# Performance work log

Hardware: AMD Instinct MI355X
Metric: run time of the kernel (lower is better)

Reference implementation:

```python
import jax, jax.numpy as jnp
import numpy as np

B, T, H, S = 2, 2048, 16, 64
EMB = H * S  # 1024


def layer_norm(x, g, b, eps=1e-5):
    mu = jnp.mean(x, axis=-1, keepdims=True)
    var = jnp.var(x, axis=-1, keepdims=True)
    return (x - mu) * jax.lax.rsqrt(var + eps) * g + b


def setup_inputs() -> dict:
    key = jax.random.key(0)
    ks = jax.random.split(key, 12)
    sc = 0.02
    return {
        "x": jax.random.normal(ks[0], (B, T, EMB), dtype=jnp.float32),
        "Wkqv": jax.random.normal(ks[1], (S, 3 * S), dtype=jnp.float32) * sc,
        "Wproj": jax.random.normal(ks[2], (EMB, EMB), dtype=jnp.float32) * sc,
        "g1": jnp.ones((EMB,), jnp.float32),
        "b1": jnp.zeros((EMB,), jnp.float32),
        "W1": jax.random.normal(ks[3], (EMB, 4 * EMB), dtype=jnp.float32) * sc,
        "bff1": jnp.zeros((4 * EMB,), jnp.float32),
        "W2": jax.random.normal(ks[4], (4 * EMB, EMB), dtype=jnp.float32) * sc,
        "bff2": jnp.zeros((EMB,), jnp.float32),
        "g2": jnp.ones((EMB,), jnp.float32),
        "b2": jnp.zeros((EMB,), jnp.float32),
    }


def reference(x, Wkqv, Wproj, g1, b1, W1, bff1, W2, bff2, g2, b2):
    Bb, Tt, _ = x.shape
    xh = x.reshape(Bb, Tt, H, S)                     # [B,T,H,S]
    kqv = jnp.einsum('bths,sd->bthd', xh, Wkqv)      # [B,T,H,3S], shared per-head weight
    k, q, v = jnp.split(kqv, 3, axis=-1)             # note order: k, q, v
    scores = jnp.einsum('bihk,bjhk->bijh', q, k) / jnp.sqrt(jnp.float32(S))
    att = jax.nn.softmax(scores, axis=2)             # softmax over key dim j
    res = jnp.einsum('btih,bihs->bths', att, v).reshape(Bb, Tt, EMB)
    mha = res @ Wproj                                # Linear(emb, emb, bias=False)
    x = layer_norm(x + mha, g1, b1)
    h = jax.nn.gelu(x @ W1 + bff1, approximate=False)
    ff = h @ W2 + bff2
    return layer_norm(x + ff, g2, b2)
```

## Files before the change

### kernel.cpp

```cpp
#include <hip/hip_runtime.h>
#include <hip/hip_bf16.h>
#include <math.h>

#define B_ 2
#define T_ 2048
#define H_ 16
#define S_ 64
#define EMB 1024
#define FF 4096
#define BT (B_*T_)
#define ROWS (B_*T_*H_)

typedef __attribute__((ext_vector_type(8))) short s16x8;
typedef __attribute__((ext_vector_type(4))) float f32x4;

struct P4 { unsigned short* p[4]; };

__device__ __forceinline__ unsigned short f2b(float f) {
    return __builtin_bit_cast(unsigned short, __float2bfloat16(f));
}
__device__ __forceinline__ float b2f(short u) {
    return __builtin_bit_cast(float, ((unsigned int)(unsigned short)u) << 16);
}

__device__ __forceinline__ void gl_lds16(const void* g, void* l) {
    __builtin_amdgcn_global_load_lds(
        (const __attribute__((address_space(1))) void*)g,
        (__attribute__((address_space(3))) void*)l, 16, 0, 0);
}

__device__ __forceinline__ f32x4 mfma16(s16x8 a, s16x8 b, f32x4 c) {
    return __builtin_amdgcn_mfma_f32_16x16x32_bf16(a, b, c, 0, 0, 0);
}

__global__ __launch_bounds__(256) void kqv_kernel(const float* __restrict__ x,
        const unsigned short* __restrict__ Wqt, unsigned short* __restrict__ K,
        unsigned short* __restrict__ Q, unsigned short* __restrict__ V) {
    const int tid = threadIdx.x;
    const int w = tid >> 6, lane = tid & 63;
    const int l15 = lane & 15, quad = lane >> 4;
    const long r0 = (long)blockIdx.x * 128 + w * 32;

    s16x8 af[2][2];
    #pragma unroll
    for (int mt = 0; mt < 2; ++mt)
        #pragma unroll
        for (int ks = 0; ks < 2; ++ks) {
            const float* xp = x + (r0 + mt*16 + l15) * 64 + ks*32 + quad*8;
            const float4 v0 = *(const float4*)xp;
            const float4 v1 = *(const float4*)(xp + 4);
            s16x8 a;
            a[0] = (short)f2b(v0.x); a[1] = (short)f2b(v0.y);
            a[2] = (short)f2b(v0.z); a[3] = (short)f2b(v0.w);
            a[4] = (short)f2b(v1.x); a[5] = (short)f2b(v1.y);
            a[6] = (short)f2b(v1.z); a[7] = (short)f2b(v1.w);
            af[mt][ks] = a;
        }

    #pragma unroll
    for (int nt = 0; nt < 12; ++nt) {
        const s16x8 b0 = *(const s16x8*)&Wqt[(nt*16 + l15)*64 + quad*8];
        const s16x8 b1 = *(const s16x8*)&Wqt[(nt*16 + l15)*64 + 32 + quad*8];
        f32x4 acc[2] = {};
        #pragma unroll
        for (int mt = 0; mt < 2; ++mt) {
            acc[mt] = mfma16(af[mt][0], b0, acc[mt]);
            acc[mt] = mfma16(af[mt][1], b1, acc[mt]);
        }
        unsigned short* dst = (nt < 4) ? K : (nt < 8) ? Q : V;
        const int c0 = (nt & 3) * 16 + l15;
        #pragma unroll
        for (int mt = 0; mt < 2; ++mt)
            #pragma unroll
            for (int r = 0; r < 4; ++r)
                dst[(r0 + mt*16 + quad*4 + r) * 64 + c0] = f2b(acc[mt][r]);
    }
}

__global__ __launch_bounds__(256) void attn_kernel(const unsigned short* __restrict__ Q,
        const unsigned short* __restrict__ K, const unsigned short* __restrict__ V,
        unsigned short* __restrict__ Po, float* __restrict__ Pl) {
    __shared__ __align__(16) unsigned short Ks[64 * 64];
    __shared__ __align__(16) unsigned short Vt[64 * 64];
    __shared__ __align__(16) unsigned short Ps[4][32 * 72];
    const int tid = threadIdx.x;
    const int w = tid >> 6, lane = tid & 63;
    const int l15 = lane & 15, quad = lane >> 4;
    const int qt = blockIdx.x;
    const int bh = blockIdx.y;
    const int sidx = blockIdx.z;
    const int b = bh >> 4, h = bh & 15;
    const long base = ((long)b * (T_ * H_) + h) * 64;
    const unsigned short* Qp = Q + base;
    const unsigned short* Kp = K + base;
    const unsigned short* Vp = V + base;
    const int q0 = qt * 128;

    s16x8 qf[2][2];
    #pragma unroll
    for (int mt = 0; mt < 2; ++mt)
        #pragma unroll
        for (int ks = 0; ks < 2; ++ks) {
            const s16x8 raw = *(const s16x8*)&Qp[(long)(q0 + w*32 + mt*16 + l15) * 1024 + ks*32 + quad*8];
            s16x8 q;
            #pragma unroll
            for (int j = 0; j < 8; ++j) q[j] = (short)f2b(b2f(raw[j]) * 0.125f);
            qf[mt][ks] = q;
        }

    s16x8 onef;
    #pragma unroll
    for (int j = 0; j < 8; ++j) onef[j] = (short)0x3F80;

    f32x4 oacc[2][4] = {};
    f32x4 lacc[2] = {};

    const int sjp = tid & 31, sd0 = (tid >> 5) * 8;
    const int kt0 = sidx * 16;
    for (int kt = kt0; kt < kt0 + 16; ++kt) {
        __syncthreads();
        #pragma unroll
        for (int i = 0; i < 2; ++i) {
            const int id = i * 256 + tid;
            const int j = id >> 3, dc = id & 7;
            const s16x8 kv = *(const s16x8*)&Kp[(long)(kt*64 + j) * 1024 + dc*8];
            *(s16x8*)&Ks[j*64 + ((dc ^ (j & 7)) * 8)] = kv;
        }
        {
            const int j0 = sjp * 2;
            const s16x8 va = *(const s16x8*)&Vp[(long)(kt*64 + j0)     * 1024 + sd0];
            const s16x8 vb = *(const s16x8*)&Vp[(long)(kt*64 + j0 + 1) * 1024 + sd0];
            const int jc = j0 >> 3;
            #pragma unroll
            for (int ii = 0; ii < 8; ++ii) {
                const unsigned int pk = (unsigned int)(unsigned short)va[ii]
                                      | ((unsigned int)(unsigned short)vb[ii] << 16);
                const int d = sd0 + ii;
                *(unsigned int*)&Vt[d*64 + ((jc ^ (d & 7)) * 8) + (j0 & 7)] = pk;
            }
        }
        __syncthreads();

        f32x4 sT[4][2] = {};
        #pragma unroll
        for (int ks = 0; ks < 2; ++ks)
            #pragma unroll
            for (int jt = 0; jt < 4; ++jt) {
                const int j = jt*16 + l15;
                const s16x8 kf = *(const s16x8*)&Ks[j*64 + (((ks*4 + quad) ^ (l15 & 7)) * 8)];
                sT[jt][0] = mfma16(kf, qf[0][ks], sT[jt][0]);
                sT[jt][1] = mfma16(kf, qf[1][ks], sT[jt][1]);
            }

        #pragma unroll
        for (int jt = 0; jt < 4; ++jt)
            #pragma unroll
            for (int qt2 = 0; qt2 < 2; ++qt2) {
                const float e0 = __expf(sT[jt][qt2][0]);
                const float e1 = __expf(sT[jt][qt2][1]);
                const float e2 = __expf(sT[jt][qt2][2]);
                const float e3 = __expf(sT[jt][qt2][3]);
                uint2 pk;
                pk.x = (unsigned int)f2b(e0) | ((unsigned int)f2b(e1) << 16);
                pk.y = (unsigned int)f2b(e2) | ((unsigned int)f2b(e3) << 16);
                *(uint2*)&Ps[w][(qt2*16 + l15)*72 + jt*16 + quad*4] = pk;
            }

        #pragma unroll
        for (int ks2 = 0; ks2 < 2; ++ks2) {
            s16x8 pf[2];
            pf[0] = *(const s16x8*)&Ps[w][(l15)*72      + ks2*32 + quad*8];
            pf[1] = *(const s16x8*)&Ps[w][(16 + l15)*72 + ks2*32 + quad*8];
            lacc[0] = mfma16(pf[0], onef, lacc[0]);
            lacc[1] = mfma16(pf[1], onef, lacc[1]);
            #pragma unroll
            for (int nt = 0; nt < 4; ++nt) {
                const int d = nt*16 + l15;
                const s16x8 vf = *(const s16x8*)&Vt[d*64 + (((ks2*4 + quad) ^ (d & 7)) * 8)];
                oacc[0][nt] = mfma16(pf[0], vf, oacc[0][nt]);
                oacc[1][nt] = mfma16(pf[1], vf, oacc[1][nt]);
            }
        }
    }

    const long po_row = (long)(sidx * 32 + bh) * T_;
    #pragma unroll
    for (int mt = 0; mt < 2; ++mt) {
        #pragma unroll
        for (int r = 0; r < 4; ++r) {
            const int t = q0 + w*32 + mt*16 + quad*4 + r;
            if (l15 == 0) Pl[po_row + t] = lacc[mt][r];
            #pragma unroll
            for (int nt = 0; nt < 4; ++nt)
                Po[(po_row + t)*64 + nt*16 + l15] = f2b(oacc[mt][nt][r]);
        }
    }
}

__global__ __launch_bounds__(256) void attn_combine(const unsigned short* __restrict__ Po,
        const float* __restrict__ Pl, unsigned short* __restrict__ res) {
    const int idx = blockIdx.x * 256 + threadIdx.x;
    const int d4 = idx & 15, bht = idx >> 4;
    const ushort4 a = ((const ushort4*)Po)[(long)bht * 16 + d4];
    const ushort4 c = ((const ushort4*)Po)[((long)bht + 32L*T_) * 16 + d4];
    const float inv = 1.f / (Pl[bht] + Pl[bht + 32*T_]);
    const int bh = bht >> 11, t = bht & (T_ - 1);
    const int b = bh >> 4, h = bh & 15;
    uint2 o;
    o.x = (unsigned int)f2b((b2f((short)a.x) + b2f((short)c.x)) * inv)
        | ((unsigned int)f2b((b2f((short)a.y) + b2f((short)c.y)) * inv) << 16);
    o.y = (unsigned int)f2b((b2f((short)a.z) + b2f((short)c.z)) * inv)
        | ((unsigned int)f2b((b2f((short)a.w) + b2f((short)c.w)) * inv) << 16);
    *(uint2*)&res[(long)(b * T_ + t) * EMB + h*64 + d4*4] = o;
}

__global__ __launch_bounds__(256) void gemm_gelu(const unsigned short* __restrict__ A,
        const unsigned short* __restrict__ Bt, const float* __restrict__ bias,
        unsigned short* __restrict__ C, int M, int N, int Kd) {
    __shared__ __align__(16) unsigned short As[128 * 32];
    __shared__ __align__(16) unsigned short Bs[128 * 32];
    const int tid = threadIdx.x;
    const int w = tid >> 6, lane = tid & 63;
    const int l15 = lane & 15, quad = lane >> 4;
    const int wm = w >> 1, wn = w & 1;
    const int bn = blockIdx.x, bm = blockIdx.y;
    const int sr = lane >> 2, skq = lane & 3;
    f32x4 acc[4][4] = {};
    const long arow = (long)(bm*128 + w*32 + sr);
    const long brow = (long)(bn*128 + w*32 + sr);

    for (int kt = 0; kt < Kd; kt += 32) {
        gl_lds16(A  + (arow     )*Kd + kt + skq*8, (char*)As + (w*32     )*64 + lane*16);
        gl_lds16(A  + (arow + 16)*Kd + kt + skq*8, (char*)As + (w*32 + 16)*64 + lane*16);
        gl_lds16(Bt + (brow     )*Kd + kt + skq*8, (char*)Bs + (w*32     )*64 + lane*16);
        gl_lds16(Bt + (brow + 16)*Kd + kt + skq*8, (char*)Bs + (w*32 + 16)*64 + lane*16);
        __syncthreads();
        s16x8 af[4], bf[4];
        #pragma unroll
        for (int mt = 0; mt < 4; ++mt)
            af[mt] = *(const s16x8*)&As[(wm*64 + mt*16 + l15)*32 + quad*8];
        #pragma unroll
        for (int nt = 0; nt < 4; ++nt)
            bf[nt] = *(const s16x8*)&Bs[(wn*64 + nt*16 + l15)*32 + quad*8];
        #pragma unroll
        for (int mt = 0; mt < 4; ++mt)
            #pragma unroll
            for (int nt = 0; nt < 4; ++nt)
                acc[mt][nt] = mfma16(af[mt], bf[nt], acc[mt][nt]);
        __syncthreads();
    }

    #pragma unroll
    for (int mt = 0; mt < 4; ++mt) {
        const int row0 = bm*128 + wm*64 + mt*16 + quad*4;
        #pragma unroll
        for (int nt = 0; nt < 4; ++nt) {
            const int col = bn*128 + wn*64 + nt*16 + l15;
            const float bv = bias[col];
            #pragma unroll
            for (int r = 0; r < 4; ++r) {
                float v = acc[mt][nt][r] + bv;
                v = 0.5f * v * (1.f + erff(v * 0.70710678118654752440f));
                C[(long)(row0 + r)*N + col] = f2b(v);
            }
        }
    }
}

__global__ __launch_bounds__(256) void gemm_splitk(const unsigned short* __restrict__ A,
        const unsigned short* __restrict__ Bt, P4 parts, int M, int N, int Kd, int Ks) {
    __shared__ __align__(16) unsigned short As[128 * 32];
    __shared__ __align__(16) unsigned short Bs[128 * 32];
    const int tid = threadIdx.x;
    const int w = tid >> 6, lane = tid & 63;
    const int l15 = lane & 15, quad = lane >> 4;
    const int wm = w >> 1, wn = w & 1;
    const int bn = blockIdx.x, bm = blockIdx.y, s = blockIdx.z;
    const int sr = lane >> 2, skq = lane & 3;
    f32x4 acc[4][4] = {};
    const long arow = (long)(bm*128 + w*32 + sr);
    const long brow = (long)(bn*128 + w*32 + sr);
    const int k0 = s * Ks;

    for (int kt = k0; kt < k0 + Ks; kt += 32) {
        gl_lds16(A  + (arow     )*Kd + kt + skq*8, (char*)As + (w*32     )*64 + lane*16);
        gl_lds16(A  + (arow + 16)*Kd + kt + skq*8, (char*)As + (w*32 + 16)*64 + lane*16);
        gl_lds16(Bt + (brow     )*Kd + kt + skq*8, (char*)Bs + (w*32     )*64 + lane*16);
        gl_lds16(Bt + (brow + 16)*Kd + kt + skq*8, (char*)Bs + (w*32 + 16)*64 + lane*16);
        __syncthreads();
        s16x8 af[4], bf[4];
        #pragma unroll
        for (int mt = 0; mt < 4; ++mt)
            af[mt] = *(const s16x8*)&As[(wm*64 + mt*16 + l15)*32 + quad*8];
        #pragma unroll
        for (int nt = 0; nt < 4; ++nt)
            bf[nt] = *(const s16x8*)&Bs[(wn*64 + nt*16 + l15)*32 + quad*8];
        #pragma unroll
        for (int mt = 0; mt < 4; ++mt)
            #pragma unroll
            for (int nt = 0; nt < 4; ++nt)
                acc[mt][nt] = mfma16(af[mt], bf[nt], acc[mt][nt]);
        __syncthreads();
    }

    unsigned short* Cp = parts.p[s];
    #pragma unroll
    for (int mt = 0; mt < 4; ++mt) {
        const int row0 = bm*128 + wm*64 + mt*16 + quad*4;
        #pragma unroll
        for (int nt = 0; nt < 4; ++nt) {
            const int col = bn*128 + wn*64 + nt*16 + l15;
            #pragma unroll
            for (int r = 0; r < 4; ++r)
                Cp[(long)(row0 + r)*N + col] = f2b(acc[mt][nt][r]);
        }
    }
}

template <int P, int XBF>
__global__ __launch_bounds__(256) void ln_kernel(const void* __restrict__ xa,
        P4 parts, const float* __restrict__ addb, const float* __restrict__ g,
        const float* __restrict__ bia, float* __restrict__ out,
        unsigned short* __restrict__ outb) {
    const int row = blockIdx.x;
    const int tid = threadIdx.x;
    float4 v;
    if (XBF) {
        const ushort4 u = ((const ushort4*)xa)[(long)row * (EMB/4) + tid];
        v.x = b2f((short)u.x); v.y = b2f((short)u.y);
        v.z = b2f((short)u.z); v.w = b2f((short)u.w);
    } else {
        v = ((const float4*)xa)[(long)row * (EMB/4) + tid];
    }
    #pragma unroll
    for (int p = 0; p < P; ++p) {
        const ushort4 u = ((const ushort4*)(parts.p[p] + (long)row * EMB))[tid];
        v.x += b2f((short)u.x); v.y += b2f((short)u.y);
        v.z += b2f((short)u.z); v.w += b2f((short)u.w);
    }
    if (addb) {
        const float4 ab = ((const float4*)addb)[tid];
        v.x += ab.x; v.y += ab.y; v.z += ab.z; v.w += ab.w;
    }
    float s = v.x + v.y + v.z + v.w;
    float ss = v.x * v.x + v.y * v.y + v.z * v.z + v.w * v.w;
    #pragma unroll
    for (int off = 32; off > 0; off >>= 1) {
        s += __shfl_down(s, off, 64);
        ss += __shfl_down(ss, off, 64);
    }
    __shared__ float ls[4], lss[4];
    __shared__ float mean_s, rstd_s;
    const int wid = tid >> 6, lane = tid & 63;
    if (lane == 0) { ls[wid] = s; lss[wid] = ss; }
    __syncthreads();
    if (tid == 0) {
        const float S0 = ls[0] + ls[1] + ls[2] + ls[3];
        const float S2 = lss[0] + lss[1] + lss[2] + lss[3];
        const float mean = S0 * (1.f / EMB);
        const float var = S2 * (1.f / EMB) - mean * mean;
        mean_s = mean;
        rstd_s = rsqrtf(var + 1e-5f);
    }
    __syncthreads();
    const float mean = mean_s, rstd = rstd_s;
    const float4 gg = ((const float4*)g)[tid];
    const float4 bb = ((const float4*)bia)[tid];
    float4 o;
    o.x = (v.x - mean) * rstd * gg.x + bb.x;
    o.y = (v.y - mean) * rstd * gg.y + bb.y;
    o.z = (v.z - mean) * rstd * gg.z + bb.z;
    o.w = (v.w - mean) * rstd * gg.w + bb.w;
    if (out) ((float4*)(out + (long)row * EMB))[tid] = o;
    if (outb) {
        unsigned short* ob = outb + (long)row * EMB + tid * 4;
        ob[0] = f2b(o.x); ob[1] = f2b(o.y); ob[2] = f2b(o.z); ob[3] = f2b(o.w);
    }
}

__global__ __launch_bounds__(256) void transp_all(const float* __restrict__ Wp,
        const float* __restrict__ W1, const float* __restrict__ W2,
        const float* __restrict__ Wq, unsigned short* __restrict__ Wpt,
        unsigned short* __restrict__ W1t, unsigned short* __restrict__ W2t,
        unsigned short* __restrict__ Wqt) {
    int id = blockIdx.x;
    const float* W; unsigned short* Wt; int Kd, N, ntx;
    if (id < 1024)      {            W = Wp; Wt = Wpt; Kd = 1024; N = 1024; ntx = 32; }
    else if (id < 5120) { id -= 1024; W = W1; Wt = W1t; Kd = 1024; N = 4096; ntx = 128; }
    else if (id < 9216) { id -= 5120; W = W2; Wt = W2t; Kd = 4096; N = 1024; ntx = 32; }
    else                { id -= 9216; W = Wq; Wt = Wqt; Kd = 64;   N = 192;  ntx = 6;  }
    __shared__ float Ts[32][33];
    const int tid = threadIdx.x;
    const int n0 = (id % ntx) * 32, k0 = (id / ntx) * 32;
    const int r = tid >> 3, c4 = (tid & 7) * 4;
    const float4 v = *(const float4*)&W[(long)(k0 + r) * N + n0 + c4];
    Ts[r][c4] = v.x; Ts[r][c4 + 1] = v.y; Ts[r][c4 + 2] = v.z; Ts[r][c4 + 3] = v.w;
    __syncthreads();
    #pragma unroll
    for (int i = 0; i < 4; ++i)
        Wt[(long)(n0 + r) * Kd + k0 + c4 + i] = f2b(Ts[c4 + i][r]);
}

extern "C" void kernel_launch(void* const* d_in, const int* in_sizes, int n_in,
                              void* d_out, int out_size, void* d_ws, size_t ws_size,
                              hipStream_t stream) {
    (void)in_sizes; (void)n_in; (void)out_size;
    const float* x     = (const float*)d_in[0];
    const float* Wkqv  = (const float*)d_in[1];
    const float* Wproj = (const float*)d_in[2];
    const float* g1    = (const float*)d_in[3];
    const float* b1    = (const float*)d_in[4];
    const float* W1    = (const float*)d_in[5];
    const float* bff1  = (const float*)d_in[6];
    const float* W2    = (const float*)d_in[7];
    const float* bff2  = (const float*)d_in[8];
    const float* g2    = (const float*)d_in[9];
    const float* b2    = (const float*)d_in[10];
    float* out = (float*)d_out;
    char* ws = (char*)d_ws;

    const size_t MB = 1u << 20;
    unsigned short* Qb   = (unsigned short*)(ws + 0 * MB);
    unsigned short* Kb   = (unsigned short*)(ws + 8 * MB);
    unsigned short* Vb   = (unsigned short*)(ws + 16 * MB);
    unsigned short* resb = (unsigned short*)(ws + 24 * MB);
    unsigned short* hb   = (unsigned short*)(ws + 8 * MB);
    unsigned short* Po   = (unsigned short*)(ws + 40 * MB);
    float*          Pl   = (float*)(ws + 56 * MB);
    unsigned short* mp0  = (unsigned short*)(ws + 40 * MB);
    unsigned short* mp1  = (unsigned short*)(ws + 48 * MB);
    unsigned short* x1b  = Qb;
    unsigned short* Wpt  = (unsigned short*)(ws + 72 * MB);
    unsigned short* W1t  = (unsigned short*)(ws + 74 * MB);
    unsigned short* W2t  = (unsigned short*)(ws + 82 * MB);
    unsigned short* Wqt  = (unsigned short*)(ws + 90 * MB);
    unsigned short* fp2  = (unsigned short*)(ws + 91 * MB);
    unsigned short* fp3  = (unsigned short*)(ws + 99 * MB);
    const bool big = ws_size >= 108 * MB;

    transp_all<<<dim3(9228), 256, 0, stream>>>(Wproj, W1, W2, Wkqv, Wpt, W1t, W2t, Wqt);

    kqv_kernel<<<dim3(ROWS/128), 256, 0, stream>>>(x, Wqt, Kb, Qb, Vb);
    attn_kernel<<<dim3(T_/128, B_*H_, 2), 256, 0, stream>>>(Qb, Kb, Vb, Po, Pl);
    attn_combine<<<dim3(32*T_*16/256), 256, 0, stream>>>(Po, Pl, resb);
    P4 mp; mp.p[0] = mp0; mp.p[1] = mp1; mp.p[2] = nullptr; mp.p[3] = nullptr;
    gemm_splitk<<<dim3(EMB/128, BT/128, 2), 256, 0, stream>>>(resb, Wpt, mp, BT, EMB, EMB, EMB/2);
    ln_kernel<2, 0><<<dim3(BT), 256, 0, stream>>>(x, mp, nullptr, g1, b1, nullptr, x1b);
    gemm_gelu<<<dim3(FF/128, BT/128), 256, 0, stream>>>(x1b, W1t, bff1, hb, BT, FF, EMB);
    if (big) {
        P4 fp; fp.p[0] = mp0; fp.p[1] = mp1; fp.p[2] = fp2; fp.p[3] = fp3;
        gemm_splitk<<<dim3(EMB/128, BT/128, 4), 256, 0, stream>>>(hb, W2t, fp, BT, EMB, FF, FF/4);
        ln_kernel<4, 1><<<dim3(BT), 256, 0, stream>>>(x1b, fp, bff2, g2, b2, out, nullptr);
    } else {
        P4 fp; fp.p[0] = mp0; fp.p[1] = mp1; fp.p[2] = nullptr; fp.p[3] = nullptr;
        gemm_splitk<<<dim3(EMB/128, BT/128, 2), 256, 0, stream>>>(hb, W2t, fp, BT, EMB, FF, FF/2);
        ln_kernel<2, 1><<<dim3(BT), 256, 0, stream>>>(x1b, fp, bff2, g2, b2, out, nullptr);
    }
}
```

Before: 374.3 us.

## Restructure attention into single-wave blocks with async double-buffered K/V staging

Adds a separate kernel that writes V in transposed layout, so attention can stream K and V^T tiles straight into LDS with global_load_lds. Each attention block becomes one wave owning 32 queries. It double-buffers 32-key tiles behind vmcnt waits instead of block-wide barriers, and normalizes the output in-kernel, which removes the split-K partial buffers and the combine kernel. The trade-offs are an extra transpose pass over V, single-wave blocks that rely on occupancy to hide latency, and no barrier between LDS writes and reads other than the vmcnt wait.

```diff
diff --git a/kernel.cpp b/kernel.cpp
--- a/kernel.cpp
+++ b/kernel.cpp
@@ -32,6 +32,9 @@
 __device__ __forceinline__ f32x4 mfma16(s16x8 a, s16x8 b, f32x4 c) {
     return __builtin_amdgcn_mfma_f32_16x16x32_bf16(a, b, c, 0, 0, 0);
 }
+
+#define WAIT_VM8 0x0F78
+#define WAIT_VM0 0x0F70
 
 __global__ __launch_bounds__(256) void kqv_kernel(const float* __restrict__ x,
         const unsigned short* __restrict__ Wqt, unsigned short* __restrict__ K,
@@ -77,35 +80,59 @@
     }
 }
 
-__global__ __launch_bounds__(256) void attn_kernel(const unsigned short* __restrict__ Q,
-        const unsigned short* __restrict__ K, const unsigned short* __restrict__ V,
-        unsigned short* __restrict__ Po, float* __restrict__ Pl) {
-    __shared__ __align__(16) unsigned short Ks[64 * 64];
-    __shared__ __align__(16) unsigned short Vt[64 * 64];
-    __shared__ __align__(16) unsigned short Ps[4][32 * 72];
-    const int tid = threadIdx.x;
-    const int w = tid >> 6, lane = tid & 63;
+__global__ __launch_bounds__(256) void vt_kernel(const unsigned short* __restrict__ V,
+        unsigned short* __restrict__ VT) {
+    __shared__ unsigned short Ts[64][72];
+    const int tid = threadIdx.x;
+    const int tt = blockIdx.x, bh = blockIdx.y;
+    const int b = bh >> 4, h = bh & 15;
+    const long vbase = ((long)b * (T_*H_) + h) * 64;
+    #pragma unroll
+    for (int i = 0; i < 2; ++i) {
+        const int id = i * 256 + tid;
+        const int tr = id >> 3, dc = (id & 7) * 8;
+        const s16x8 v = *(const s16x8*)&V[vbase + (long)(tt*64 + tr)*1024 + dc];
+        *(s16x8*)&Ts[tr][dc] = v;
+    }
+    __syncthreads();
+    #pragma unroll
+    for (int i = 0; i < 2; ++i) {
+        const int id = i * 256 + tid;
+        const int d = id >> 3, tc = (id & 7) * 8;
+        s16x8 o;
+        #pragma unroll
+        for (int j = 0; j < 8; ++j) o[j] = (short)Ts[tc + j][d];
+        *(s16x8*)&VT[((long)bh*64 + d)*2048 + tt*64 + tc] = o;
+    }
+}
+
+__global__ __launch_bounds__(64, 2) void attn_kernel(const unsigned short* __restrict__ Q,
+        const unsigned short* __restrict__ K, const unsigned short* __restrict__ VT,
+        unsigned short* __restrict__ res) {
+    __shared__ __align__(16) unsigned short Kbuf[2][2][32*32];
+    __shared__ __align__(16) unsigned short Vbuf[2][64*32];
+    __shared__ __align__(16) unsigned short Ps[32*36];
+    const int lane = threadIdx.x;
     const int l15 = lane & 15, quad = lane >> 4;
-    const int qt = blockIdx.x;
-    const int bh = blockIdx.y;
-    const int sidx = blockIdx.z;
+    const int bid = blockIdx.x;
+    const int qt = bid & 63, bh = bid >> 6;
     const int b = bh >> 4, h = bh & 15;
-    const long base = ((long)b * (T_ * H_) + h) * 64;
+    const long base = ((long)b * (T_*H_) + h) * 64;
     const unsigned short* Qp = Q + base;
     const unsigned short* Kp = K + base;
-    const unsigned short* Vp = V + base;
-    const int q0 = qt * 128;
+    const unsigned short* Vp = VT + (long)bh * 64 * 2048;
+    const int q0 = qt * 32;
 
     s16x8 qf[2][2];
     #pragma unroll
-    for (int mt = 0; mt < 2; ++mt)
+    for (int qq = 0; qq < 2; ++qq)
         #pragma unroll
         for (int ks = 0; ks < 2; ++ks) {
-            const s16x8 raw = *(const s16x8*)&Qp[(long)(q0 + w*32 + mt*16 + l15) * 1024 + ks*32 + quad*8];
+            const s16x8 raw = *(const s16x8*)&Qp[(long)(q0 + qq*16 + l15)*1024 + ks*32 + quad*8];
             s16x8 q;
             #pragma unroll
             for (int j = 0; j < 8; ++j) q[j] = (short)f2b(b2f(raw[j]) * 0.125f);
-            qf[mt][ks] = q;
+            qf[qq][ks] = q;
         }
 
     s16x8 onef;
@@ -115,103 +142,81 @@
     f32x4 oacc[2][4] = {};
     f32x4 lacc[2] = {};
 
-    const int sjp = tid & 31, sd0 = (tid >> 5) * 8;
-    const int kt0 = sidx * 16;
-    for (int kt = kt0; kt < kt0 + 16; ++kt) {
-        __syncthreads();
-        #pragma unroll
-        for (int i = 0; i < 2; ++i) {
-            const int id = i * 256 + tid;
-            const int j = id >> 3, dc = id & 7;
-            const s16x8 kv = *(const s16x8*)&Kp[(long)(kt*64 + j) * 1024 + dc*8];
-            *(s16x8*)&Ks[j*64 + ((dc ^ (j & 7)) * 8)] = kv;
-        }
-        {
-            const int j0 = sjp * 2;
-            const s16x8 va = *(const s16x8*)&Vp[(long)(kt*64 + j0)     * 1024 + sd0];
-            const s16x8 vb = *(const s16x8*)&Vp[(long)(kt*64 + j0 + 1) * 1024 + sd0];
-            const int jc = j0 >> 3;
-            #pragma unroll
-            for (int ii = 0; ii < 8; ++ii) {
-                const unsigned int pk = (unsigned int)(unsigned short)va[ii]
-                                      | ((unsigned int)(unsigned short)vb[ii] << 16);
-                const int d = sd0 + ii;
-                *(unsigned int*)&Vt[d*64 + ((jc ^ (d & 7)) * 8) + (j0 & 7)] = pk;
-            }
-        }
-        __syncthreads();
-
-        f32x4 sT[4][2] = {};
+    const int j16 = lane >> 2;
+    const int c8  = (lane & 3) * 8;
+
+    auto stage = [&](int bufi, int kt) {
+        const unsigned short* kg = Kp + (long)(kt*32) * 1024;
+        char* kl = (char*)&Kbuf[bufi][0][0];
+        gl_lds16(kg + (long)j16*1024 + c8,           kl +    0 + lane*16);
+        gl_lds16(kg + (long)(j16+16)*1024 + c8,      kl + 1024 + lane*16);
+        gl_lds16(kg + (long)j16*1024 + 32 + c8,      kl + 2048 + lane*16);
+        gl_lds16(kg + (long)(j16+16)*1024 + 32 + c8, kl + 3072 + lane*16);
+        const unsigned short* vg = Vp + kt*32 + c8;
+        char* vl = (char*)&Vbuf[bufi][0];
+        gl_lds16(vg + (long)(j16     )*2048, vl +    0 + lane*16);
+        gl_lds16(vg + (long)(j16 + 16)*2048, vl + 1024 + lane*16);
+        gl_lds16(vg + (long)(j16 + 32)*2048, vl + 2048 + lane*16);
+        gl_lds16(vg + (long)(j16 + 48)*2048, vl + 3072 + lane*16);
+    };
+
+    auto compute = [&](int bufi) {
+        f32x4 sT[2][2] = {};
         #pragma unroll
         for (int ks = 0; ks < 2; ++ks)
             #pragma unroll
-            for (int jt = 0; jt < 4; ++jt) {
-                const int j = jt*16 + l15;
-                const s16x8 kf = *(const s16x8*)&Ks[j*64 + (((ks*4 + quad) ^ (l15 & 7)) * 8)];
+            for (int jt = 0; jt < 2; ++jt) {
+                const s16x8 kf = *(const s16x8*)&Kbuf[bufi][ks][(jt*16 + l15)*32 + quad*8];
                 sT[jt][0] = mfma16(kf, qf[0][ks], sT[jt][0]);
                 sT[jt][1] = mfma16(kf, qf[1][ks], sT[jt][1]);
             }
-
-        #pragma unroll
-        for (int jt = 0; jt < 4; ++jt)
-            #pragma unroll
-            for (int qt2 = 0; qt2 < 2; ++qt2) {
-                const float e0 = __expf(sT[jt][qt2][0]);
-                const float e1 = __expf(sT[jt][qt2][1]);
-                const float e2 = __expf(sT[jt][qt2][2]);
-                const float e3 = __expf(sT[jt][qt2][3]);
+        #pragma unroll
+        for (int jt = 0; jt < 2; ++jt)
+            #pragma unroll
+            for (int qq = 0; qq < 2; ++qq) {
                 uint2 pk;
-                pk.x = (unsigned int)f2b(e0) | ((unsigned int)f2b(e1) << 16);
-                pk.y = (unsigned int)f2b(e2) | ((unsigned int)f2b(e3) << 16);
-                *(uint2*)&Ps[w][(qt2*16 + l15)*72 + jt*16 + quad*4] = pk;
+                pk.x = (unsigned int)f2b(__expf(sT[jt][qq][0]))
+                     | ((unsigned int)f2b(__expf(sT[jt][qq][1])) << 16);
+                pk.y = (unsigned int)f2b(__expf(sT[jt][qq][2]))
+                     | ((unsigned int)f2b(__expf(sT[jt][qq][3])) << 16);
+                *(uint2*)&Ps[(qq*16 + l15)*36 + jt*16 + quad*4] = pk;
             }
-
-        #pragma unroll
-        for (int ks2 = 0; ks2 < 2; ++ks2) {
-            s16x8 pf[2];
-            pf[0] = *(const s16x8*)&Ps[w][(l15)*72      + ks2*32 + quad*8];
-            pf[1] = *(const s16x8*)&Ps[w][(16 + l15)*72 + ks2*32 + quad*8];
-            lacc[0] = mfma16(pf[0], onef, lacc[0]);
-            lacc[1] = mfma16(pf[1], onef, lacc[1]);
-            #pragma unroll
-            for (int nt = 0; nt < 4; ++nt) {
-                const int d = nt*16 + l15;
-                const s16x8 vf = *(const s16x8*)&Vt[d*64 + (((ks2*4 + quad) ^ (d & 7)) * 8)];
-                oacc[0][nt] = mfma16(pf[0], vf, oacc[0][nt]);
-                oacc[1][nt] = mfma16(pf[1], vf, oacc[1][nt]);
-            }
-        }
-    }
-
-    const long po_row = (long)(sidx * 32 + bh) * T_;
-    #pragma unroll
-    for (int mt = 0; mt < 2; ++mt) {
+        s16x8 pf[2];
+        #pragma unroll
+        for (int qq = 0; qq < 2; ++qq) {
+            pf[qq] = *(const s16x8*)&Ps[(qq*16 + l15)*36 + quad*8];
+            lacc[qq] = mfma16(pf[qq], onef, lacc[qq]);
+        }
+        #pragma unroll
+        for (int nt = 0; nt < 4; ++nt) {
+            const s16x8 vf = *(const s16x8*)&Vbuf[bufi][(nt*16 + l15)*32 + quad*8];
+            oacc[0][nt] = mfma16(pf[0], vf, oacc[0][nt]);
+            oacc[1][nt] = mfma16(pf[1], vf, oacc[1][nt]);
+        }
+    };
+
+    stage(0, 0);
+    for (int kt = 0; kt < 63; ++kt) {
+        stage((kt + 1) & 1, kt + 1);
+        __builtin_amdgcn_s_waitcnt(WAIT_VM8);
+        __builtin_amdgcn_sched_barrier(0);
+        compute(kt & 1);
+    }
+    __builtin_amdgcn_s_waitcnt(WAIT_VM0);
+    __builtin_amdgcn_sched_barrier(0);
+    compute(1);
+
+    #pragma unroll
+    for (int qq = 0; qq < 2; ++qq)
         #pragma unroll
         for (int r = 0; r < 4; ++r) {
-            const int t = q0 + w*32 + mt*16 + quad*4 + r;
-            if (l15 == 0) Pl[po_row + t] = lacc[mt][r];
+            const float inv = 1.f / lacc[qq][r];
+            const int t = q0 + qq*16 + quad*4 + r;
             #pragma unroll
             for (int nt = 0; nt < 4; ++nt)
-                Po[(po_row + t)*64 + nt*16 + l15] = f2b(oacc[mt][nt][r]);
-        }
-    }
-}
-
-__global__ __launch_bounds__(256) void attn_combine(const unsigned short* __restrict__ Po,
-        const float* __restrict__ Pl, unsigned short* __restrict__ res) {
-    const int idx = blockIdx.x * 256 + threadIdx.x;
-    const int d4 = idx & 15, bht = idx >> 4;
-    const ushort4 a = ((const ushort4*)Po)[(long)bht * 16 + d4];
-    const ushort4 c = ((const ushort4*)Po)[((long)bht + 32L*T_) * 16 + d4];
-    const float inv = 1.f / (Pl[bht] + Pl[bht + 32*T_]);
-    const int bh = bht >> 11, t = bht & (T_ - 1);
-    const int b = bh >> 4, h = bh & 15;
-    uint2 o;
-    o.x = (unsigned int)f2b((b2f((short)a.x) + b2f((short)c.x)) * inv)
-        | ((unsigned int)f2b((b2f((short)a.y) + b2f((short)c.y)) * inv) << 16);
-    o.y = (unsigned int)f2b((b2f((short)a.z) + b2f((short)c.z)) * inv)
-        | ((unsigned int)f2b((b2f((short)a.w) + b2f((short)c.w)) * inv) << 16);
-    *(uint2*)&res[(long)(b * T_ + t) * EMB + h*64 + d4*4] = o;
+                res[((long)(b*T_ + t))*EMB + h*64 + nt*16 + l15] =
+                    f2b(oacc[qq][nt][r] * inv);
+        }
 }
 
 __global__ __launch_bounds__(256) void gemm_gelu(const unsigned short* __restrict__ A,
@@ -425,8 +430,7 @@
     unsigned short* Vb   = (unsigned short*)(ws + 16 * MB);
     unsigned short* resb = (unsigned short*)(ws + 24 * MB);
     unsigned short* hb   = (unsigned short*)(ws + 8 * MB);
-    unsigned short* Po   = (unsigned short*)(ws + 40 * MB);
-    float*          Pl   = (float*)(ws + 56 * MB);
+    unsigned short* VTb  = (unsigned short*)(ws + 40 * MB);
     unsigned short* mp0  = (unsigned short*)(ws + 40 * MB);
     unsigned short* mp1  = (unsigned short*)(ws + 48 * MB);
     unsigned short* x1b  = Qb;
@@ -441,8 +445,8 @@
     transp_all<<<dim3(9228), 256, 0, stream>>>(Wproj, W1, W2, Wkqv, Wpt, W1t, W2t, Wqt);
 
     kqv_kernel<<<dim3(ROWS/128), 256, 0, stream>>>(x, Wqt, Kb, Qb, Vb);
-    attn_kernel<<<dim3(T_/128, B_*H_, 2), 256, 0, stream>>>(Qb, Kb, Vb, Po, Pl);
-    attn_combine<<<dim3(32*T_*16/256), 256, 0, stream>>>(Po, Pl, resb);
+    vt_kernel<<<dim3(T_/64, B_*H_), 256, 0, stream>>>(Vb, VTb);
+    attn_kernel<<<dim3(2048), 64, 0, stream>>>(Qb, Kb, VTb, resb);
     P4 mp; mp.p[0] = mp0; mp.p[1] = mp1; mp.p[2] = nullptr; mp.p[3] = nullptr;
     gemm_splitk<<<dim3(EMB/128, BT/128, 2), 256, 0, stream>>>(resb, Wpt, mp, BT, EMB, EMB, EMB/2);
     ln_kernel<2, 0><<<dim3(BT), 256, 0, stream>>>(x, mp, nullptr, g1, b1, nullptr, x1b);
```

Result: faster. 361.3 us (-3.5%).
